# Performance work log

Hardware: AMD Instinct MI355X
Metric: run time of the kernel (lower is better)

The kernel has to match this reference:

```python
import jax, jax.numpy as jnp
import numpy as np

SCALE_FACTOR = 8.0  # sqrt(head_dim=64)

def setup_inputs() -> dict:
    key = jax.random.key(0)
    kq, kk, kv = jax.random.split(key, 3)
    BH, S, D = 64, 2048, 64  # batch*heads, seq_len, head_dim
    q = jax.random.normal(kq, (BH, S, D), dtype=jnp.float32)
    k = jax.random.normal(kk, (BH, S, D), dtype=jnp.float32)
    v = jax.random.normal(kv, (BH, S, D), dtype=jnp.float32)
    return {"q": q, "k": k, "v": v}

def reference(q, k, v):
    # qk = q @ k^T, scaled, softmax over keys, (dropout p=0 == identity), @ v
    scores = jnp.einsum("bqd,bkd->bqk", q, k) / SCALE_FACTOR  # [BH, S, S]
    attn = jax.nn.softmax(scores, axis=-1)
    out = jnp.einsum("bqk,bkd->bqd", attn, v)  # [BH, S, D]
    return out
```

## Files before the change

### kernel.cpp

```cpp
#include <hip/hip_runtime.h>
#include <hip/hip_bf16.h>


typedef __attribute__((ext_vector_type(8))) short short8;
typedef __attribute__((ext_vector_type(4))) short short4v;
typedef __attribute__((ext_vector_type(4))) float float4v;

#define S_LEN 2048
#define D_DIM 64
#define BH_N  64
#define LOG2E 1.4426950408889634f
#define CLF   (0.125f * LOG2E)

__device__ __forceinline__ unsigned int fpack2_fast(float a, float b) {
    unsigned int ua = __builtin_bit_cast(unsigned int, a) + 0x8000u;
    unsigned int ub = __builtin_bit_cast(unsigned int, b) + 0x8000u;
    return __builtin_amdgcn_perm(ub, ua, 0x07060302);
}
__device__ __forceinline__ unsigned int fpack2_trunc(float a, float b) {
    return __builtin_amdgcn_perm(__builtin_bit_cast(unsigned int, b),
                                 __builtin_bit_cast(unsigned int, a),
                                 0x07060302);
}
__device__ __forceinline__ void load16_lds(const unsigned short* g, unsigned short* l) {
    __builtin_amdgcn_global_load_lds(
        (const __attribute__((address_space(1))) unsigned int*)g,
        (__attribute__((address_space(3))) unsigned int*)l,
        16, 0, 0);
}

__global__ void __launch_bounds__(256) prep(const float* __restrict__ k,
                                            const float* __restrict__ v,
                                            unsigned short* __restrict__ kbf,
                                            unsigned short* __restrict__ vt) {
    __shared__ unsigned short T[64 * 66];
    const int b = blockIdx.x;
    const int t = threadIdx.x;
    if (b & 1) {
        const int kb = b >> 1;
        const size_t i = ((size_t)kb * 256 + t) * 16;
        #pragma unroll
        for (int j = 0; j < 2; ++j) {
            const float4 a0 = *(const float4*)(k + i + j * 8);
            const float4 a1 = *(const float4*)(k + i + j * 8 + 4);
            uint4 o;
            o.x = fpack2_fast(a0.x, a0.y); o.y = fpack2_fast(a0.z, a0.w);
            o.z = fpack2_fast(a1.x, a1.y); o.w = fpack2_fast(a1.z, a1.w);
            *(uint4*)(kbf + i + j * 8) = o;
        }
        return;
    }
    const int idx = b >> 1;
    const int kt = idx & 31, bh = idx >> 5;
    const float* Vg = v + ((size_t)bh * S_LEN + kt * 64) * D_DIM;
    #pragma unroll
    for (int it = 0; it < 4; ++it) {
        const int row = it * 16 + (t >> 4);
        const int col = (t & 15) * 4;
        const float4 f = *(const float4*)(Vg + row * 64 + col);
        unsigned int* p = (unsigned int*)&T[row * 66 + col];
        p[0] = fpack2_fast(f.x, f.y);
        p[1] = fpack2_fast(f.z, f.w);
    }
    __syncthreads();
    const int d  = t >> 2;
    const int cg = t & 3;
    unsigned int w8[8];
    #pragma unroll
    for (int cc = 0; cc < 2; ++cc) {
        const int c   = cg * 2 + cc;
        const int kb0 = (c >> 2) * 32 + (c & 3) * 4;
        w8[cc*4+0] = __builtin_amdgcn_perm(T[(kb0+ 1)*66+d], T[(kb0+ 0)*66+d], 0x05040100);
        w8[cc*4+1] = __builtin_amdgcn_perm(T[(kb0+ 3)*66+d], T[(kb0+ 2)*66+d], 0x05040100);
        w8[cc*4+2] = __builtin_amdgcn_perm(T[(kb0+17)*66+d], T[(kb0+16)*66+d], 0x05040100);
        w8[cc*4+3] = __builtin_amdgcn_perm(T[(kb0+19)*66+d], T[(kb0+18)*66+d], 0x05040100);
    }
    unsigned short* outp = vt + ((size_t)bh * 64 + d) * S_LEN + kt * 64 + cg * 16;
    uint4 o0; o0.x = w8[0]; o0.y = w8[1]; o0.z = w8[2]; o0.w = w8[3];
    uint4 o1; o1.x = w8[4]; o1.y = w8[5]; o1.z = w8[6]; o1.w = w8[7];
    *(uint4*)(outp)     = o0;
    *(uint4*)(outp + 8) = o1;
}

__global__ void __launch_bounds__(128, 2) attn_fwd9(
        const float* __restrict__ q, const unsigned short* __restrict__ kbf,
        const unsigned short* __restrict__ vt, float* __restrict__ out) {
    __shared__ __align__(16) unsigned short Klds[2][64 * 64];
    __shared__ __align__(16) unsigned short Vlds[2][64 * 64];

    const int tid  = threadIdx.x;
    const int lane = tid & 63;
    const int wave = tid >> 6;
    const int l16  = lane & 15;
    const int quad = lane >> 4;
    const int rsw  = l16 & 7;

    const int bh    = blockIdx.y;
    const int qbase = blockIdx.x * 128;

    const unsigned short* Kb = kbf + (size_t)bh * S_LEN * D_DIM;
    const unsigned short* Vb = vt  + (size_t)bh * D_DIM * S_LEN;

    short8 qf[4][2];
    #pragma unroll
    for (int s = 0; s < 4; ++s) {
        const int qg = qbase + wave * 64 + s * 16 + l16;
        const float* Qr = q + ((size_t)bh * S_LEN + qg) * D_DIM;
        #pragma unroll
        for (int h = 0; h < 2; ++h) {
            const float4 a = *(const float4*)(Qr + h * 32 + quad * 8);
            const float4 b = *(const float4*)(Qr + h * 32 + quad * 8 + 4);
            uint4 w;
            w.x = fpack2_fast(a.x * CLF, a.y * CLF);
            w.y = fpack2_fast(a.z * CLF, a.w * CLF);
            w.z = fpack2_fast(b.x * CLF, b.y * CLF);
            w.w = fpack2_fast(b.z * CLF, b.w * CLF);
            qf[s][h] = __builtin_bit_cast(short8, w);
        }
    }

    const int srow0  = wave * 32 + (lane >> 3);
    const int schunk = (lane & 7) ^ (lane >> 3);
    const int dsoff  = wave * 2048 + lane * 8;
    const int p0     = (quad ^ rsw) * 8;

    float4v acc[4][4];
    #pragma unroll
    for (int s = 0; s < 4; ++s)
        #pragma unroll
        for (int dt = 0; dt < 4; ++dt) acc[s][dt] = (float4v){0.f, 0.f, 0.f, 0.f};
    float l_acc[4] = {0.f, 0.f, 0.f, 0.f};

    auto stage = [&](int kt, int buf) {
        #pragma unroll
        for (int ss = 0; ss < 4; ++ss) {
            const int row = srow0 + ss * 8;
            load16_lds(Kb + ((size_t)(kt * 64 + row)) * 64 + schunk * 8,
                       &Klds[buf][dsoff + ss * 512]);
            load16_lds(Vb + (size_t)row * S_LEN + kt * 64 + schunk * 8,
                       &Vlds[buf][dsoff + ss * 512]);
        }
    };

    auto tile = [&](int buf) {
        short8 kf[4][2];
        #pragma unroll
        for (int ks = 0; ks < 4; ++ks) {
            const unsigned short* kr = &Klds[buf][(ks * 16 + l16) * 64];
            kf[ks][0] = *(const short8*)(kr + p0);
            kf[ks][1] = *(const short8*)(kr + (p0 ^ 32));
        }
        short8 pf[4][2];
        #pragma unroll
        for (int s = 0; s < 4; ++s) {
            float4v st[4];
            #pragma unroll
            for (int ks = 0; ks < 4; ++ks) {
                float4v z = (float4v){0.f, 0.f, 0.f, 0.f};
                z = __builtin_amdgcn_mfma_f32_16x16x32_bf16(kf[ks][0], qf[s][0], z, 0, 0, 0);
                z = __builtin_amdgcn_mfma_f32_16x16x32_bf16(kf[ks][1], qf[s][1], z, 0, 0, 0);
                st[ks] = z;
            }
            #pragma unroll
            for (int w = 0; w < 2; ++w) {
                const float e0 = __builtin_amdgcn_exp2f(st[2*w][0]);
                const float e1 = __builtin_amdgcn_exp2f(st[2*w][1]);
                const float e2 = __builtin_amdgcn_exp2f(st[2*w][2]);
                const float e3 = __builtin_amdgcn_exp2f(st[2*w][3]);
                const float f0 = __builtin_amdgcn_exp2f(st[2*w+1][0]);
                const float f1 = __builtin_amdgcn_exp2f(st[2*w+1][1]);
                const float f2 = __builtin_amdgcn_exp2f(st[2*w+1][2]);
                const float f3 = __builtin_amdgcn_exp2f(st[2*w+1][3]);
                l_acc[s] += ((e0 + e1) + (e2 + e3)) + ((f0 + f1) + (f2 + f3));
                uint4 u;
                u.x = fpack2_trunc(e0, e1); u.y = fpack2_trunc(e2, e3);
                u.z = fpack2_trunc(f0, f1); u.w = fpack2_trunc(f2, f3);
                pf[s][w] = __builtin_bit_cast(short8, u);
            }
        }
        #pragma unroll
        for (int dt = 0; dt < 4; ++dt) {
            const unsigned short* vrow = &Vlds[buf][(dt * 16 + l16) * 64];
            const short8 vf0 = *(const short8*)(vrow + p0);
            const short8 vf1 = *(const short8*)(vrow + (p0 ^ 32));
            #pragma unroll
            for (int s = 0; s < 4; ++s) {
                acc[s][dt] = __builtin_amdgcn_mfma_f32_16x16x32_bf16(vf0, pf[s][0], acc[s][dt], 0, 0, 0);
                acc[s][dt] = __builtin_amdgcn_mfma_f32_16x16x32_bf16(vf1, pf[s][1], acc[s][dt], 0, 0, 0);
            }
        }
    };

    stage(0, 0);
    #pragma unroll 1
    for (int kt = 0; kt < S_LEN / 64; kt += 2) {
        __syncthreads();
        stage(kt + 1, 1);
        tile(0);
        __syncthreads();
        if (kt + 2 < S_LEN / 64) stage(kt + 2, 0);
        tile(1);
    }

    #pragma unroll
    for (int s = 0; s < 4; ++s) {
        float l = l_acc[s];
        l += __shfl_xor(l, 16, 64);
        l += __shfl_xor(l, 32, 64);
        const float inv = 1.0f / l;
        const int qg = qbase + wave * 64 + s * 16 + l16;
        float* Or = out + ((size_t)bh * S_LEN + qg) * D_DIM;
        #pragma unroll
        for (int dt = 0; dt < 4; ++dt) {
            float4 o;
            o.x = acc[s][dt][0] * inv; o.y = acc[s][dt][1] * inv;
            o.z = acc[s][dt][2] * inv; o.w = acc[s][dt][3] * inv;
            *(float4*)(Or + dt * 16 + quad * 4) = o;
        }
    }
}

#define KSTRIDE 72
__global__ void __launch_bounds__(256) attn_fwd(
        const float* __restrict__ q, const float* __restrict__ k,
        const float* __restrict__ v, float* __restrict__ out) {
    __shared__ __align__(16) unsigned short Klds[64 * KSTRIDE];
    __shared__ __align__(16) unsigned short Vlds[64 * KSTRIDE];
    const int tid  = threadIdx.x;
    const int lane = tid & 63;
    const int wave = tid >> 6;
    const int l16  = lane & 15;
    const int quad = lane >> 4;
    const int bh    = blockIdx.y;
    const int qg    = blockIdx.x * 64 + wave * 16 + l16;
    const float* Qr = q + ((size_t)bh * S_LEN + qg) * D_DIM;
    const float* Kb = k + (size_t)bh * S_LEN * D_DIM;
    const float* Vb = v + (size_t)bh * S_LEN * D_DIM;
    short8 qf[2];
    #pragma unroll
    for (int h = 0; h < 2; ++h) {
        const float4 a = *(const float4*)(Qr + h * 32 + quad * 8);
        const float4 b = *(const float4*)(Qr + h * 32 + quad * 8 + 4);
        uint4 w;
        w.x = fpack2_fast(a.x * CLF, a.y * CLF);
        w.y = fpack2_fast(a.z * CLF, a.w * CLF);
        w.z = fpack2_fast(b.x * CLF, b.y * CLF);
        w.w = fpack2_fast(b.z * CLF, b.w * CLF);
        qf[h] = __builtin_bit_cast(short8, w);
    }
    float4v acc[4];
    #pragma unroll
    for (int dt = 0; dt < 4; ++dt) acc[dt] = (float4v){0.f, 0.f, 0.f, 0.f};
    float l_acc = 0.f;
    for (int kt = 0; kt < S_LEN / 64; ++kt) {
        __syncthreads();
        {
            const float* Kg = Kb + (size_t)kt * 64 * D_DIM;
            #pragma unroll
            for (int i = 0; i < 4; ++i) {
                const int idx = tid + i * 256;
                const int row = idx >> 4;
                const int col = (idx & 15) << 2;
                const float4 f = *(const float4*)(Kg + row * 64 + col);
                uint2 w; w.x = fpack2_fast(f.x, f.y); w.y = fpack2_fast(f.z, f.w);
                *(uint2*)(&Klds[row * KSTRIDE + col]) = w;
            }
        }
        {
            const float* Vg = Vb + (size_t)kt * 64 * D_DIM;
            #pragma unroll
            for (int it = 0; it < 2; ++it) {
                const int rp   = (tid & 15) + (it << 4);
                const int cg   = tid >> 4;
                const int row0 = rp * 2;
                const int col  = cg * 4;
                const float4 a = *(const float4*)(Vg + row0 * 64 + col);
                const float4 b = *(const float4*)(Vg + (row0 + 1) * 64 + col);
                *(unsigned int*)(&Vlds[(col + 0) * KSTRIDE + row0]) = fpack2_fast(a.x, b.x);
                *(unsigned int*)(&Vlds[(col + 1) * KSTRIDE + row0]) = fpack2_fast(a.y, b.y);
                *(unsigned int*)(&Vlds[(col + 2) * KSTRIDE + row0]) = fpack2_fast(a.z, b.z);
                *(unsigned int*)(&Vlds[(col + 3) * KSTRIDE + row0]) = fpack2_fast(a.w, b.w);
            }
        }
        __syncthreads();
        float4v st[4];
        #pragma unroll
        for (int ks = 0; ks < 4; ++ks) {
            const unsigned short* kr = &Klds[(ks * 16 + l16) * KSTRIDE + quad * 8];
            const short8 kf0 = *(const short8*)(kr);
            const short8 kf1 = *(const short8*)(kr + 32);
            float4v z = (float4v){0.f, 0.f, 0.f, 0.f};
            z = __builtin_amdgcn_mfma_f32_16x16x32_bf16(kf0, qf[0], z, 0, 0, 0);
            z = __builtin_amdgcn_mfma_f32_16x16x32_bf16(kf1, qf[1], z, 0, 0, 0);
            st[ks] = z;
        }
        short4v pf[4];
        #pragma unroll
        for (int ks = 0; ks < 4; ++ks) {
            const float p0 = __builtin_amdgcn_exp2f(st[ks][0]);
            const float p1 = __builtin_amdgcn_exp2f(st[ks][1]);
            const float p2 = __builtin_amdgcn_exp2f(st[ks][2]);
            const float p3 = __builtin_amdgcn_exp2f(st[ks][3]);
            l_acc += (p0 + p1) + (p2 + p3);
            uint2 u; u.x = fpack2_trunc(p0, p1); u.y = fpack2_trunc(p2, p3);
            pf[ks] = __builtin_bit_cast(short4v, u);
        }
        #pragma unroll
        for (int dt = 0; dt < 4; ++dt) {
            const unsigned short* vr = &Vlds[(dt * 16 + l16) * KSTRIDE + quad * 4];
            #pragma unroll
            for (int ks = 0; ks < 4; ++ks) {
                const short4v vf = *(const short4v*)(vr + ks * 16);
                acc[dt] = __builtin_amdgcn_mfma_f32_16x16x16bf16_1k(vf, pf[ks], acc[dt], 0, 0, 0);
            }
        }
    }
    float l = l_acc;
    l += __shfl_xor(l, 16, 64);
    l += __shfl_xor(l, 32, 64);
    const float inv = 1.0f / l;
    float* Or = out + ((size_t)bh * S_LEN + qg) * D_DIM;
    #pragma unroll
    for (int dt = 0; dt < 4; ++dt) {
        float4 o;
        o.x = acc[dt][0] * inv; o.y = acc[dt][1] * inv;
        o.z = acc[dt][2] * inv; o.w = acc[dt][3] * inv;
        *(float4*)(Or + dt * 16 + quad * 4) = o;
    }
}

extern "C" void kernel_launch(void* const* d_in, const int* in_sizes, int n_in,
                              void* d_out, int out_size, void* d_ws, size_t ws_size,
                              hipStream_t stream) {
    const float* q = (const float*)d_in[0];
    const float* k = (const float*)d_in[1];
    const float* v = (const float*)d_in[2];
    float* out = (float*)d_out;
    const size_t need = (size_t)2 * BH_N * S_LEN * D_DIM * sizeof(unsigned short);
    if (ws_size >= need) {
        unsigned short* kbf = (unsigned short*)d_ws;
        unsigned short* vtp = kbf + (size_t)BH_N * S_LEN * D_DIM;
        prep<<<dim3(4096), 256, 0, stream>>>(k, v, kbf, vtp);
        attn_fwd9<<<dim3(S_LEN / 128, BH_N), 128, 0, stream>>>(q, kbf, vtp, out);
    } else {
        attn_fwd<<<dim3(S_LEN / 64, BH_N), 256, 0, stream>>>(q, k, v, out);
    }
}
```

Before: 203.3 us.

## Split each KV tile across wave pairs and reduce partial outputs via LDS

The attention kernel now runs 256 threads per block, and two waves share each 64-row query group. Each wave of a pair handles one half of the 64 keys in every KV tile, so the per-wave score MFMAs, exp work and PV MFMAs are halved and staging is spread over four waves. At the end, the partial output accumulators and row sums from one half are written to LDS, reusing the K/V buffers, and the other half adds them before normalising. This buys more waves per CU for latency hiding, at the cost of an extra LDS reduction with syncs and the same staging traffic spread over more threads.

```diff
diff --git a/kernel.cpp b/kernel.cpp
--- a/kernel.cpp
+++ b/kernel.cpp
@@ -82,15 +82,18 @@
     *(uint4*)(outp + 8) = o1;
 }
 
-__global__ void __launch_bounds__(128, 2) attn_fwd9(
+__global__ void __launch_bounds__(256, 4) attn_fwd10(
         const float* __restrict__ q, const unsigned short* __restrict__ kbf,
         const unsigned short* __restrict__ vt, float* __restrict__ out) {
     __shared__ __align__(16) unsigned short Klds[2][64 * 64];
     __shared__ __align__(16) unsigned short Vlds[2][64 * 64];
+    __shared__ float Lp[2][4][16];
 
     const int tid  = threadIdx.x;
     const int lane = tid & 63;
     const int wave = tid >> 6;
+    const int qg    = wave >> 1;
+    const int khalf = wave & 1;
     const int l16  = lane & 15;
     const int quad = lane >> 4;
     const int rsw  = l16 & 7;
@@ -104,8 +107,8 @@
     short8 qf[4][2];
     #pragma unroll
     for (int s = 0; s < 4; ++s) {
-        const int qg = qbase + wave * 64 + s * 16 + l16;
-        const float* Qr = q + ((size_t)bh * S_LEN + qg) * D_DIM;
+        const int qrow = qbase + qg * 64 + s * 16 + l16;
+        const float* Qr = q + ((size_t)bh * S_LEN + qrow) * D_DIM;
         #pragma unroll
         for (int h = 0; h < 2; ++h) {
             const float4 a = *(const float4*)(Qr + h * 32 + quad * 8);
@@ -119,10 +122,11 @@
         }
     }
 
-    const int srow0  = wave * 32 + (lane >> 3);
+    const int srow0  = wave * 16 + (lane >> 3);
     const int schunk = (lane & 7) ^ (lane >> 3);
-    const int dsoff  = wave * 2048 + lane * 8;
+    const int dsoff  = wave * 1024 + lane * 8;
     const int p0     = (quad ^ rsw) * 8;
+    const int pvx    = khalf << 5;
 
     float4v acc[4][4];
     #pragma unroll
@@ -133,7 +137,7 @@
 
     auto stage = [&](int kt, int buf) {
         #pragma unroll
-        for (int ss = 0; ss < 4; ++ss) {
+        for (int ss = 0; ss < 2; ++ss) {
             const int row = srow0 + ss * 8;
             load16_lds(Kb + ((size_t)(kt * 64 + row)) * 64 + schunk * 8,
                        &Klds[buf][dsoff + ss * 512]);
@@ -143,51 +147,45 @@
     };
 
     auto tile = [&](int buf) {
-        short8 kf[4][2];
-        #pragma unroll
-        for (int ks = 0; ks < 4; ++ks) {
-            const unsigned short* kr = &Klds[buf][(ks * 16 + l16) * 64];
-            kf[ks][0] = *(const short8*)(kr + p0);
-            kf[ks][1] = *(const short8*)(kr + (p0 ^ 32));
-        }
-        short8 pf[4][2];
+        short8 kf[2][2];
+        #pragma unroll
+        for (int ksi = 0; ksi < 2; ++ksi) {
+            const unsigned short* kr = &Klds[buf][((khalf * 2 + ksi) * 16 + l16) * 64];
+            kf[ksi][0] = *(const short8*)(kr + p0);
+            kf[ksi][1] = *(const short8*)(kr + (p0 ^ 32));
+        }
+        short8 pf[4];
         #pragma unroll
         for (int s = 0; s < 4; ++s) {
-            float4v st[4];
-            #pragma unroll
-            for (int ks = 0; ks < 4; ++ks) {
+            float4v st[2];
+            #pragma unroll
+            for (int ksi = 0; ksi < 2; ++ksi) {
                 float4v z = (float4v){0.f, 0.f, 0.f, 0.f};
-                z = __builtin_amdgcn_mfma_f32_16x16x32_bf16(kf[ks][0], qf[s][0], z, 0, 0, 0);
-                z = __builtin_amdgcn_mfma_f32_16x16x32_bf16(kf[ks][1], qf[s][1], z, 0, 0, 0);
-                st[ks] = z;
-            }
-            #pragma unroll
-            for (int w = 0; w < 2; ++w) {
-                const float e0 = __builtin_amdgcn_exp2f(st[2*w][0]);
-                const float e1 = __builtin_amdgcn_exp2f(st[2*w][1]);
-                const float e2 = __builtin_amdgcn_exp2f(st[2*w][2]);
-                const float e3 = __builtin_amdgcn_exp2f(st[2*w][3]);
-                const float f0 = __builtin_amdgcn_exp2f(st[2*w+1][0]);
-                const float f1 = __builtin_amdgcn_exp2f(st[2*w+1][1]);
-                const float f2 = __builtin_amdgcn_exp2f(st[2*w+1][2]);
-                const float f3 = __builtin_amdgcn_exp2f(st[2*w+1][3]);
-                l_acc[s] += ((e0 + e1) + (e2 + e3)) + ((f0 + f1) + (f2 + f3));
-                uint4 u;
-                u.x = fpack2_trunc(e0, e1); u.y = fpack2_trunc(e2, e3);
-                u.z = fpack2_trunc(f0, f1); u.w = fpack2_trunc(f2, f3);
-                pf[s][w] = __builtin_bit_cast(short8, u);
-            }
+                z = __builtin_amdgcn_mfma_f32_16x16x32_bf16(kf[ksi][0], qf[s][0], z, 0, 0, 0);
+                z = __builtin_amdgcn_mfma_f32_16x16x32_bf16(kf[ksi][1], qf[s][1], z, 0, 0, 0);
+                st[ksi] = z;
+            }
+            const float e0 = __builtin_amdgcn_exp2f(st[0][0]);
+            const float e1 = __builtin_amdgcn_exp2f(st[0][1]);
+            const float e2 = __builtin_amdgcn_exp2f(st[0][2]);
+            const float e3 = __builtin_amdgcn_exp2f(st[0][3]);
+            const float f0 = __builtin_amdgcn_exp2f(st[1][0]);
+            const float f1 = __builtin_amdgcn_exp2f(st[1][1]);
+            const float f2 = __builtin_amdgcn_exp2f(st[1][2]);
+            const float f3 = __builtin_amdgcn_exp2f(st[1][3]);
+            l_acc[s] += ((e0 + e1) + (e2 + e3)) + ((f0 + f1) + (f2 + f3));
+            uint4 u;
+            u.x = fpack2_trunc(e0, e1); u.y = fpack2_trunc(e2, e3);
+            u.z = fpack2_trunc(f0, f1); u.w = fpack2_trunc(f2, f3);
+            pf[s] = __builtin_bit_cast(short8, u);
         }
         #pragma unroll
         for (int dt = 0; dt < 4; ++dt) {
             const unsigned short* vrow = &Vlds[buf][(dt * 16 + l16) * 64];
-            const short8 vf0 = *(const short8*)(vrow + p0);
-            const short8 vf1 = *(const short8*)(vrow + (p0 ^ 32));
-            #pragma unroll
-            for (int s = 0; s < 4; ++s) {
-                acc[s][dt] = __builtin_amdgcn_mfma_f32_16x16x32_bf16(vf0, pf[s][0], acc[s][dt], 0, 0, 0);
-                acc[s][dt] = __builtin_amdgcn_mfma_f32_16x16x32_bf16(vf1, pf[s][1], acc[s][dt], 0, 0, 0);
-            }
+            const short8 vf = *(const short8*)(vrow + (p0 ^ pvx));
+            #pragma unroll
+            for (int s = 0; s < 4; ++s)
+                acc[s][dt] = __builtin_amdgcn_mfma_f32_16x16x32_bf16(vf, pf[s], acc[s][dt], 0, 0, 0);
         }
     };
 
@@ -202,20 +200,43 @@
         tile(1);
     }
 
+    float lw[4];
     #pragma unroll
     for (int s = 0; s < 4; ++s) {
         float l = l_acc[s];
         l += __shfl_xor(l, 16, 64);
         l += __shfl_xor(l, 32, 64);
-        const float inv = 1.0f / l;
-        const int qg = qbase + wave * 64 + s * 16 + l16;
-        float* Or = out + ((size_t)bh * S_LEN + qg) * D_DIM;
-        #pragma unroll
-        for (int dt = 0; dt < 4; ++dt) {
-            float4 o;
-            o.x = acc[s][dt][0] * inv; o.y = acc[s][dt][1] * inv;
-            o.z = acc[s][dt][2] * inv; o.w = acc[s][dt][3] * inv;
-            *(float4*)(Or + dt * 16 + quad * 4) = o;
+        lw[s] = l;
+    }
+    __syncthreads();
+    if (khalf) {
+        float* dst = qg ? (float*)&Vlds[0][0] : (float*)&Klds[0][0];
+        #pragma unroll
+        for (int s = 0; s < 4; ++s) {
+            if (quad == 0) Lp[qg][s][l16] = lw[s];
+            #pragma unroll
+            for (int dt = 0; dt < 4; ++dt)
+                *(float4v*)(dst + (s * 16 + l16) * 64 + dt * 16 + quad * 4) = acc[s][dt];
+        }
+    }
+    __syncthreads();
+    if (!khalf) {
+        const float* src = qg ? (const float*)&Vlds[0][0] : (const float*)&Klds[0][0];
+        #pragma unroll
+        for (int s = 0; s < 4; ++s) {
+            const float inv = 1.0f / (lw[s] + Lp[qg][s][l16]);
+            const int qrow = qbase + qg * 64 + s * 16 + l16;
+            float* Or = out + ((size_t)bh * S_LEN + qrow) * D_DIM;
+            #pragma unroll
+            for (int dt = 0; dt < 4; ++dt) {
+                const float4v part = *(const float4v*)(src + (s * 16 + l16) * 64 + dt * 16 + quad * 4);
+                float4 o;
+                o.x = (acc[s][dt][0] + part[0]) * inv;
+                o.y = (acc[s][dt][1] + part[1]) * inv;
+                o.z = (acc[s][dt][2] + part[2]) * inv;
+                o.w = (acc[s][dt][3] + part[3]) * inv;
+                *(float4*)(Or + dt * 16 + quad * 4) = o;
+            }
         }
     }
 }
@@ -341,7 +362,7 @@
         unsigned short* kbf = (unsigned short*)d_ws;
         unsigned short* vtp = kbf + (size_t)BH_N * S_LEN * D_DIM;
         prep<<<dim3(4096), 256, 0, stream>>>(k, v, kbf, vtp);
-        attn_fwd9<<<dim3(S_LEN / 128, BH_N), 128, 0, stream>>>(q, kbf, vtp, out);
+        attn_fwd10<<<dim3(S_LEN / 128, BH_N), 256, 0, stream>>>(q, kbf, vtp, out);
     } else {
         attn_fwd<<<dim3(S_LEN / 64, BH_N), 256, 0, stream>>>(q, k, v, out);
     }
```

After: 600.2 us. +195.2%, slower.
